# Kernel optimization log

Hardware: AMD Instinct MI355X
Metric: run time of the kernel (lower is better)

Reference implementation:

```python
import jax, jax.numpy as jnp
import numpy as np

EPS = 1e-8
CMAP_SHARPNESS = 100.0  # sigmoid sharpness in contact_map_of_m_to_n


def setup_inputs() -> dict:
    key = jax.random.key(0)
    k1, k2, k3, k4 = jax.random.split(key, 4)
    N, M, V, F = 8192, 4096, 2048, 2048
    obj_points = jax.random.normal(k1, (N, 3), jnp.float32)
    sr_points = 0.8 * jax.random.normal(k2, (M, 3), jnp.float32)
    verts = 0.8 * jax.random.normal(k3, (V, 3), jnp.float32)
    faces = jax.random.randint(k4, (F, 3), 0, V)
    tri = verts[faces]                                   # [F,3,3]
    fn = jnp.cross(tri[:, 1] - tri[:, 0], tri[:, 2] - tri[:, 0])
    face_normals = fn / (jnp.linalg.norm(fn, axis=-1, keepdims=True) + EPS)
    return {"obj_points": obj_points, "sr_points": sr_points,
            "verts": verts, "faces": faces, "face_normals": face_normals}


def _ray_triangle_hits(origins, dirs, tri, face_normals):
    """Plane-intersection + barycentric inside test. Returns [F,N] bool hits (t>=0)."""
    v0 = tri[:, 0]                                       # [F,3]
    denom = jnp.einsum('fc,nc->fn', face_normals, dirs)  # [F,N]
    safe = jnp.where(jnp.abs(denom) < EPS, EPS, denom)
    num = (jnp.einsum('fc,fc->f', face_normals, v0)[:, None]
           - jnp.einsum('fc,nc->fn', face_normals, origins))
    t = num / safe                                       # [F,N]
    p = origins[None, :, :] + t[..., None] * dirs[None, :, :]  # [F,N,3]
    inside = jnp.ones(t.shape, dtype=bool)
    for i in range(3):  # fixed 3 triangle edges
        vi = tri[:, i]
        vj = tri[:, (i + 1) % 3]
        c = jnp.cross((vj - vi)[:, None, :], p - vi[:, None, :])  # [F,N,3]
        inside = inside & (jnp.einsum('fnc,fc->fn', c, face_normals) >= 0.0)
    return inside & (t >= 0.0) & (jnp.abs(denom) >= EPS)


def reference(obj_points, sr_points, verts, faces, face_normals):
    # get_NN: brute-force nearest sampled hand point for each object point
    d2 = jnp.sum((obj_points[:, None, :] - sr_points[None, :, :]) ** 2, axis=-1)  # [N,M]
    nn_idx = jnp.argmin(d2, axis=1)                      # [N]
    trg_pts = sr_points[nn_idx]                          # batched_index_select
    ray_dirs = trg_pts - obj_points                      # [N,3]
    tri = verts[faces]                                   # v[f] -> [F,3,3]
    hits = _ray_triangle_hits(obj_points, ray_dirs, tri, face_normals)  # [F,N]
    hit_number = jnp.sum(hits.astype(jnp.int32), axis=0)
    interior_mask = (hit_number % 2) != 0                # [N]
    # torch.norm(trg_pts[mask] - obj_points[mask]) == Frobenius norm over masked rows
    pen_dist = jnp.sqrt(jnp.sum(jnp.where(interior_mask[:, None], ray_dirs, 0.0) ** 2))
    # contact_map_of_m_to_n: per-obj-point contact value from NN distance
    nn_dist = jnp.sqrt(jnp.min(d2, axis=1) + EPS)
    cmap = 1.0 - 2.0 * (jax.nn.sigmoid(CMAP_SHARPNESS * nn_dist) - 0.5)
    return pen_dist, cmap
```

## Files before the change

kernel.cpp:

```cpp
#include <hip/hip_runtime.h>
#include <hip/hip_bf16.h>
#include <math.h>

#define EPSF 1e-8f

constexpr int N_OBJ  = 8192;
constexpr int M_SR   = 4096;
constexpr int N_FACE = 2048;

constexpr size_t OFF_CAND = (size_t)N_FACE * 16 * sizeof(float);
constexpr size_t OFF_PEN  = OFF_CAND + 2ull * N_OBJ * sizeof(float4);
constexpr size_t OFF_BM   = OFF_PEN + (size_t)N_OBJ * sizeof(float);

constexpr int SR_HALF = M_SR / 2;
constexpr int SRTILE  = 1024;
constexpr int NN_PPW  = 4;
constexpr int NN_PPB  = NN_PPW * 4;
constexpr int NN_NBLK = (N_OBJ / NN_PPB) * 2;
constexpr int SETUP_BLKS = N_FACE / 256;

__global__ __launch_bounds__(256) void d1_nn_setup(
    const float* __restrict__ obj, const float* __restrict__ srp,
    const float* __restrict__ verts, const int* __restrict__ faces,
    const float* __restrict__ fnorm, float* __restrict__ fd,
    float4* __restrict__ cand)
{
    const int b   = blockIdx.x;
    const int tid = threadIdx.x;

    if (b >= NN_NBLK) {
        int f = (b - NN_NBLK) * 256 + tid;
        int i0 = faces[3 * f + 0], i1 = faces[3 * f + 1], i2 = faces[3 * f + 2];
        float ax = verts[3 * i0 + 0], ay = verts[3 * i0 + 1], az = verts[3 * i0 + 2];
        float bx = verts[3 * i1 + 0], by = verts[3 * i1 + 1], bz = verts[3 * i1 + 2];
        float cx = verts[3 * i2 + 0], cy = verts[3 * i2 + 1], cz = verts[3 * i2 + 2];
        float fx = fnorm[3 * f + 0], fy = fnorm[3 * f + 1], fz = fnorm[3 * f + 2];
        float nf = fx * ax + fy * ay + fz * az;

        float e0x = bx - ax, e0y = by - ay, e0z = bz - az;
        float g0x = fy * e0z - fz * e0y, g0y = fz * e0x - fx * e0z, g0z = fx * e0y - fy * e0x;
        float h0  = g0x * ax + g0y * ay + g0z * az;
        float e1x = cx - bx, e1y = cy - by, e1z = cz - bz;
        float g1x = fy * e1z - fz * e1y, g1y = fz * e1x - fx * e1z, g1z = fx * e1y - fy * e1x;
        float h1  = g1x * bx + g1y * by + g1z * bz;
        float e2x = ax - cx, e2y = ay - cy, e2z = az - cz;
        float g2x = fy * e2z - fz * e2y, g2y = fz * e2x - fx * e2z, g2z = fx * e2y - fy * e2x;
        float h2  = g2x * cx + g2y * cy + g2z * cz;

        float* o = fd + f * 16;
        o[0] = fx;  o[1] = fy;  o[2] = fz;  o[3] = nf;
        o[4] = g0x; o[5] = g0y; o[6] = g0z; o[7] = h0;
        o[8] = g1x; o[9] = g1y; o[10] = g1z; o[11] = h1;
        o[12] = g2x; o[13] = g2y; o[14] = g2z; o[15] = h2;
        return;
    }

    __shared__ float4 s4[SRTILE];
    const int half = b & 1;
    const int ptg  = b >> 1;
    const int w    = tid >> 6;
    const int lane = tid & 63;
    const int pbase = ptg * NN_PPB + w * NN_PPW;
    const float* __restrict__ sbase = srp + 3 * half * SR_HALF;

    float ox[NN_PPW], oy[NN_PPW], oz[NN_PPW], best[NN_PPW];
    int bi[NN_PPW];
#pragma unroll
    for (int q = 0; q < NN_PPW; ++q) {
        int n = pbase + q;
        ox[q] = obj[3 * n]; oy[q] = obj[3 * n + 1]; oz[q] = obj[3 * n + 2];
        best[q] = 3.4e38f; bi[q] = 0;
    }

    for (int t0 = 0; t0 < SR_HALF; t0 += SRTILE) {
        __syncthreads();
        for (int i = tid; i < SRTILE; i += 256) {
            float sx = sbase[3 * (t0 + i) + 0];
            float sy = sbase[3 * (t0 + i) + 1];
            float sz = sbase[3 * (t0 + i) + 2];
            s4[i] = make_float4(sx, sy, sz, sx * sx + sy * sy + sz * sz);
        }
        __syncthreads();
#pragma unroll 4
        for (int j = 0; j < SRTILE / 64; ++j) {
            int s = j * 64 + lane;
            float4 v = s4[s];
#pragma unroll
            for (int q = 0; q < NN_PPW; ++q) {
                float m = v.w - 2.0f * (ox[q] * v.x + oy[q] * v.y + oz[q] * v.z);
                if (m < best[q]) { best[q] = m; bi[q] = t0 + s; }
            }
        }
    }
    for (int off = 1; off < 64; off <<= 1) {
#pragma unroll
        for (int q = 0; q < NN_PPW; ++q) {
            float od = __shfl_xor(best[q], off);
            int   oi = __shfl_xor(bi[q], off);
            if (od < best[q] || (od == best[q] && oi < bi[q])) { best[q] = od; bi[q] = oi; }
        }
    }
    if (lane == 0) {
#pragma unroll
        for (int q = 0; q < NN_PPW; ++q) {
            int n  = pbase + q;
            int gi = half * SR_HALF + bi[q];
            float dx = srp[3 * gi + 0] - ox[q];
            float dy = srp[3 * gi + 1] - oy[q];
            float dz = srp[3 * gi + 2] - oz[q];
            cand[half * N_OBJ + n] = make_float4(dx, dy, dz, best[q]);
        }
    }
}

constexpr int FK_SPLITS = 64;
constexpr int FK_PTBLK  = N_OBJ / 256;
constexpr int FK_NBLK   = FK_PTBLK * FK_SPLITS;

__global__ __launch_bounds__(256, 4) void d2_face(
    const float* __restrict__ obj, const float* __restrict__ fd,
    const float4* __restrict__ cand, float* __restrict__ out,
    float* __restrict__ pend2, unsigned long long* __restrict__ bm)
{
    const int tid   = threadIdx.x;
    const int w     = tid >> 6;
    const int lane  = tid & 63;
    const int fs    = blockIdx.x & (FK_SPLITS - 1);
    const int ptblk = blockIdx.x >> 6;
    const int p     = ptblk * 256 + tid;

    float4 c0 = cand[p];
    float4 c1 = cand[N_OBJ + p];
    const bool tb = c1.w < c0.w;
    const float dx = tb ? c1.x : c0.x;
    const float dy = tb ? c1.y : c0.y;
    const float dz = tb ? c1.z : c0.z;
    const float m  = tb ? c1.w : c0.w;

    const float ox = obj[3 * p], oy = obj[3 * p + 1], oz = obj[3 * p + 2];

    if (fs == 0) {
        float d2 = m + (ox * ox + oy * oy + oz * oz);
        pend2[p] = d2;
        out[1 + p] = 2.0f / (1.0f + expf(100.0f * sqrtf(d2 + EPSF)));
    }

    const float4* __restrict__ c4 = (const float4*)fd + (size_t)(fs * 32) * 4;

    int cnt = 0;
#pragma unroll 4
    for (int j = 0; j < 32; ++j) {
        float4 q0 = c4[4 * j + 0];
        float den = q0.x * dx + q0.y * dy + q0.z * dz;
        float num = q0.w - (q0.x * ox + q0.y * oy + q0.z * oz);
        float Px  = den * ox + num * dx;
        float Py  = den * oy + num * dy;
        float Pz  = den * oz + num * dz;
        bool pos = den >= 0.0f;

        float4 q1 = c4[4 * j + 1];
        bool ok0 = ((q1.x * Px + q1.y * Py + q1.z * Pz - den * q1.w) >= 0.0f) == pos;
        float4 q2 = c4[4 * j + 2];
        bool ok1 = ((q2.x * Px + q2.y * Py + q2.z * Pz - den * q2.w) >= 0.0f) == pos;
        float4 q3 = c4[4 * j + 3];
        bool ok2 = ((q3.x * Px + q3.y * Py + q3.z * Pz - den * q3.w) >= 0.0f) == pos;

        bool tok = (num >= 0.0f) == pos;
        bool aok = fabsf(den) >= EPSF;
        cnt += (ok0 & ok1 & ok2 & tok & aok) ? 1 : 0;
    }

    unsigned long long msk = __ballot((cnt & 1) != 0);
    if (lane == 0) bm[(size_t)(ptblk * 4 + w) * 64 + fs] = msk;
}

__global__ __launch_bounds__(256) void d3_fin(
    const float* __restrict__ pend2, const unsigned long long* __restrict__ bm,
    float* __restrict__ out)
{
    __shared__ float wsum[4];
    const int t    = threadIdx.x;
    const int col  = t >> 1;
    const int half = t & 1;

    const ulonglong2* __restrict__ q2 =
        (const ulonglong2*)(bm + (size_t)col * 64) + half * 16;
    unsigned long long x = 0;
#pragma unroll
    for (int k = 0; k < 16; ++k) { ulonglong2 v = q2[k]; x ^= v.x ^ v.y; }
    x ^= __shfl_xor(x, 1);

    unsigned int bits = (unsigned int)(x >> (half * 32));
    const float4* __restrict__ p4 = (const float4*)(pend2 + (size_t)col * 64 + half * 32);
    float s = 0.0f;
#pragma unroll
    for (int k = 0; k < 8; ++k) {
        float4 v = p4[k];
        unsigned int nib = (bits >> (4 * k)) & 0xFu;
        s += (nib & 1u) ? v.x : 0.0f;
        s += (nib & 2u) ? v.y : 0.0f;
        s += (nib & 4u) ? v.z : 0.0f;
        s += (nib & 8u) ? v.w : 0.0f;
    }

    for (int off = 1; off < 64; off <<= 1) s += __shfl_xor(s, off);
    if ((t & 63) == 0) wsum[t >> 6] = s;
    __syncthreads();
    if (t == 0) out[0] = sqrtf(wsum[0] + wsum[1] + wsum[2] + wsum[3]);
}

extern "C" void kernel_launch(void* const* d_in, const int* in_sizes, int n_in,
                              void* d_out, int out_size, void* d_ws, size_t ws_size,
                              hipStream_t stream)
{
    const float* obj   = (const float*)d_in[0];
    const float* srp   = (const float*)d_in[1];
    const float* verts = (const float*)d_in[2];
    const int*   faces = (const int*)d_in[3];
    const float* fnorm = (const float*)d_in[4];
    float*       out   = (float*)d_out;

    float*              fd    = (float*)d_ws;
    float4*             cand  = (float4*)((char*)d_ws + OFF_CAND);
    float*              pend2 = (float*)((char*)d_ws + OFF_PEN);
    unsigned long long* bm    = (unsigned long long*)((char*)d_ws + OFF_BM);

    d1_nn_setup<<<NN_NBLK + SETUP_BLKS, 256, 0, stream>>>(obj, srp, verts, faces, fnorm, fd, cand);
    d2_face<<<FK_NBLK, 256, 0, stream>>>(obj, fd, cand, out, pend2, bm);
    d3_fin<<<1, 256, 0, stream>>>(pend2, bm, out);
}
```

Measured before the change: 37.13 us.

## Drop shared-memory tiling in NN search and double face-kernel split count

The nearest-neighbour phase stops staging hand points into LDS with block barriers. Each lane now reads its point straight from global memory with an unaligned float4 load, guarding the final element against reading past the buffer, and computes the exact squared distance rather than the expanded dot-product form. The face-intersection kernel splits the faces into 128 groups instead of 64 and drops its occupancy hint, and the final reduction reads the larger bitmask array. This is meant to remove barrier and LDS overhead and to expose more parallelism, at the cost of more global loads, more blocks and more partial bitmasks to XOR together.

```diff
diff --git a/kernel.cpp b/kernel.cpp
--- a/kernel.cpp
+++ b/kernel.cpp
@@ -13,7 +13,6 @@
 constexpr size_t OFF_BM   = OFF_PEN + (size_t)N_OBJ * sizeof(float);
 
 constexpr int SR_HALF = M_SR / 2;
-constexpr int SRTILE  = 1024;
 constexpr int NN_PPW  = 4;
 constexpr int NN_PPB  = NN_PPW * 4;
 constexpr int NN_NBLK = (N_OBJ / NN_PPB) * 2;
@@ -55,13 +54,12 @@
         return;
     }
 
-    __shared__ float4 s4[SRTILE];
     const int half = b & 1;
     const int ptg  = b >> 1;
     const int w    = tid >> 6;
     const int lane = tid & 63;
     const int pbase = ptg * NN_PPB + w * NN_PPW;
-    const float* __restrict__ sbase = srp + 3 * half * SR_HALF;
+    const int sgbase = half * SR_HALF;
 
     float ox[NN_PPW], oy[NN_PPW], oz[NN_PPW], best[NN_PPW];
     int bi[NN_PPW];
@@ -72,26 +70,25 @@
         best[q] = 3.4e38f; bi[q] = 0;
     }
 
-    for (int t0 = 0; t0 < SR_HALF; t0 += SRTILE) {
-        __syncthreads();
-        for (int i = tid; i < SRTILE; i += 256) {
-            float sx = sbase[3 * (t0 + i) + 0];
-            float sy = sbase[3 * (t0 + i) + 1];
-            float sz = sbase[3 * (t0 + i) + 2];
-            s4[i] = make_float4(sx, sy, sz, sx * sx + sy * sy + sz * sz);
-        }
-        __syncthreads();
 #pragma unroll 4
-        for (int j = 0; j < SRTILE / 64; ++j) {
-            int s = j * 64 + lane;
-            float4 v = s4[s];
-#pragma unroll
-            for (int q = 0; q < NN_PPW; ++q) {
-                float m = v.w - 2.0f * (ox[q] * v.x + oy[q] * v.y + oz[q] * v.z);
-                if (m < best[q]) { best[q] = m; bi[q] = t0 + s; }
-            }
-        }
-    }
+    for (int j = 0; j < SR_HALF / 64; ++j) {
+        const int sg = sgbase + j * 64 + lane;
+        float4 v;
+        if (j == SR_HALF / 64 - 1 && half == 1 && lane == 63) {
+            v.x = srp[3 * sg]; v.y = srp[3 * sg + 1]; v.z = srp[3 * sg + 2]; v.w = 0.0f;
+        } else {
+            v = *(const float4*)(srp + 3 * sg);
+        }
+#pragma unroll
+        for (int q = 0; q < NN_PPW; ++q) {
+            float dx = ox[q] - v.x;
+            float dy = oy[q] - v.y;
+            float dz = oz[q] - v.z;
+            float d2 = dx * dx + dy * dy + dz * dz;
+            if (d2 < best[q]) { best[q] = d2; bi[q] = sg; }
+        }
+    }
+
     for (int off = 1; off < 64; off <<= 1) {
 #pragma unroll
         for (int q = 0; q < NN_PPW; ++q) {
@@ -104,7 +101,7 @@
 #pragma unroll
         for (int q = 0; q < NN_PPW; ++q) {
             int n  = pbase + q;
-            int gi = half * SR_HALF + bi[q];
+            int gi = bi[q];
             float dx = srp[3 * gi + 0] - ox[q];
             float dy = srp[3 * gi + 1] - oy[q];
             float dz = srp[3 * gi + 2] - oz[q];
@@ -113,11 +110,11 @@
     }
 }
 
-constexpr int FK_SPLITS = 64;
+constexpr int FK_SPLITS = 128;
 constexpr int FK_PTBLK  = N_OBJ / 256;
 constexpr int FK_NBLK   = FK_PTBLK * FK_SPLITS;
 
-__global__ __launch_bounds__(256, 4) void d2_face(
+__global__ __launch_bounds__(256) void d2_face(
     const float* __restrict__ obj, const float* __restrict__ fd,
     const float4* __restrict__ cand, float* __restrict__ out,
     float* __restrict__ pend2, unsigned long long* __restrict__ bm)
@@ -126,7 +123,7 @@
     const int w     = tid >> 6;
     const int lane  = tid & 63;
     const int fs    = blockIdx.x & (FK_SPLITS - 1);
-    const int ptblk = blockIdx.x >> 6;
+    const int ptblk = blockIdx.x >> 7;
     const int p     = ptblk * 256 + tid;
 
     float4 c0 = cand[p];
@@ -140,16 +137,15 @@
     const float ox = obj[3 * p], oy = obj[3 * p + 1], oz = obj[3 * p + 2];
 
     if (fs == 0) {
-        float d2 = m + (ox * ox + oy * oy + oz * oz);
-        pend2[p] = d2;
-        out[1 + p] = 2.0f / (1.0f + expf(100.0f * sqrtf(d2 + EPSF)));
-    }
-
-    const float4* __restrict__ c4 = (const float4*)fd + (size_t)(fs * 32) * 4;
+        pend2[p] = m;
+        out[1 + p] = 2.0f / (1.0f + expf(100.0f * sqrtf(m + EPSF)));
+    }
+
+    const float4* __restrict__ c4 = (const float4*)fd + (size_t)(fs * 16) * 4;
 
     int cnt = 0;
-#pragma unroll 4
-    for (int j = 0; j < 32; ++j) {
+#pragma unroll 8
+    for (int j = 0; j < 16; ++j) {
         float4 q0 = c4[4 * j + 0];
         float den = q0.x * dx + q0.y * dy + q0.z * dz;
         float num = q0.w - (q0.x * ox + q0.y * oy + q0.z * oz);
@@ -171,7 +167,7 @@
     }
 
     unsigned long long msk = __ballot((cnt & 1) != 0);
-    if (lane == 0) bm[(size_t)(ptblk * 4 + w) * 64 + fs] = msk;
+    if (lane == 0) bm[(size_t)(ptblk * 4 + w) * FK_SPLITS + fs] = msk;
 }
 
 __global__ __launch_bounds__(256) void d3_fin(
@@ -184,10 +180,10 @@
     const int half = t & 1;
 
     const ulonglong2* __restrict__ q2 =
-        (const ulonglong2*)(bm + (size_t)col * 64) + half * 16;
+        (const ulonglong2*)(bm + (size_t)col * FK_SPLITS) + half * 32;
     unsigned long long x = 0;
 #pragma unroll
-    for (int k = 0; k < 16; ++k) { ulonglong2 v = q2[k]; x ^= v.x ^ v.y; }
+    for (int k = 0; k < 32; ++k) { ulonglong2 v = q2[k]; x ^= v.x ^ v.y; }
     x ^= __shfl_xor(x, 1);
 
     unsigned int bits = (unsigned int)(x >> (half * 32));
```

After: 38.16 us. +2.8%, slower.
